# Kernel optimization log

Measured on AMD Instinct MI355X. Metric: run time of the kernel, lower is better.

The kernel has to match this reference:

```python
import jax, jax.numpy as jnp
import numpy as np

B = 64                      # batch_size: number of candidate elements
N_PER = 100_000             # observations per candidate
DATA = B * N_PER            # data_size
EPS = 1e-6
INV_ROOT_2PI = 1.0 / np.sqrt(2.0 * np.pi)

def _deg2dist(deg):
    # chord distance on unit sphere subtended by angle deg
    return 2.0 * np.sin(np.radians(deg) / 2.0)

THRESH_DEG = 1.0
THRESH_S2_MIN = np.float32(_deg2dist(10.0 / 3600.0) ** 2)
THRESH_S2_MAX = np.float32(_deg2dist(THRESH_DEG) ** 2)
LOG_THRESH_S2_RANGE = np.float32(np.log(THRESH_S2_MAX / THRESH_S2_MIN))


def setup_inputs() -> dict:
    key = jax.random.key(0)
    k1, k2, k3, k4, k5 = jax.random.split(key, 5)
    u_obs = jax.random.normal(k1, (DATA, 3), dtype=jnp.float32)
    u_obs = u_obs / jnp.linalg.norm(u_obs, axis=-1, keepdims=True)   # unit directions
    # predicted directions = observed + small perturbation so some obs fall inside threshold
    u_pred = u_obs + 0.01 * jax.random.normal(k2, (DATA, 3), dtype=jnp.float32)
    u_pred = u_pred / jnp.linalg.norm(u_pred, axis=-1, keepdims=True)
    mag_obs = 18.0 + jax.random.normal(k3, (DATA,), dtype=jnp.float32)
    R_elt = 0.001 + 0.004 * jax.random.uniform(k4, (B,), dtype=jnp.float32)  # resolution param
    thresh_s2_ = jax.random.uniform(k5, (B,), dtype=jnp.float32)             # trainable, in [0,1]
    seg_ids = jnp.repeat(jnp.arange(B, dtype=jnp.int32), N_PER)              # ragged row_lengths -> segment ids
    return {"u_pred": u_pred, "R_elt": R_elt, "u_obs": u_obs,
            "mag_obs": mag_obs, "thresh_s2_": thresh_s2_, "seg_ids": seg_ids}


def reference(u_pred, R_elt, u_obs, mag_obs, thresh_s2_, seg_ids):
    # threshold transform (get_thresh_s2)
    thresh_s2_elt = THRESH_S2_MIN * jnp.exp(thresh_s2_ * LOG_THRESH_S2_RANGE)    # [B]
    thresh_all = thresh_s2_elt[seg_ids]                                          # [DATA]

    # calc_dist: squared chord distance + threshold mask
    du = u_pred - u_obs
    s2 = jnp.sum(du * du, axis=-1)                                               # [DATA]
    is_close = s2 < thresh_all                                                   # bool [DATA]
    mask = is_close.astype(s2.dtype)
    v = s2 / thresh_all                                                          # in [0,1] on close obs

    # cond_pdf_dist: exponential-family pdf conditional on a hit (q_miss = 1)
    lam_elt = 0.5 * thresh_s2_elt / (R_elt * R_elt)                              # [B]
    lam = lam_elt[seg_ids]                                                       # [DATA]
    log_q_hit = -lam * v + jnp.log(lam) - jnp.log1p(-jnp.exp(-lam))              # log(e^{-lam v} lam / (1 - e^{-lam}))

    # mag_standardize: per-candidate mean/std over close observations -> z-score
    n_close = jax.ops.segment_sum(mask, seg_ids, num_segments=B, indices_are_sorted=True)
    n_safe = jnp.maximum(n_close, 1.0)
    sum_m = jax.ops.segment_sum(mask * mag_obs, seg_ids, num_segments=B, indices_are_sorted=True)
    sum_m2 = jax.ops.segment_sum(mask * mag_obs * mag_obs, seg_ids, num_segments=B, indices_are_sorted=True)
    mu = sum_m / n_safe                                                          # [B]
    var = jnp.maximum(sum_m2 / n_safe - mu * mu, EPS)
    sigma_hat = jnp.sqrt(var)                                                    # [B]

    z = (mag_obs - mu[seg_ids]) / sigma_hat[seg_ids]                             # [DATA]
    log_p_mag = jnp.log(INV_ROOT_2PI / sigma_hat[seg_ids]) - 0.5 * z * z

    # per-candidate score: segment-sum of log conditional densities on close obs
    score = jax.ops.segment_sum(mask * (log_q_hit + log_p_mag), seg_ids,
                                num_segments=B, indices_are_sorted=True)         # [B]
    return score
```

## Files before the change

kernel.cpp:

```cpp
#include <hip/hip_runtime.h>
#include <math.h>


#define BLOCK 128
#define WAVES (BLOCK / 64)
#define SEG_BLOCKS 16
#define WAVES_PER_SEG (SEG_BLOCKS * WAVES)
#define OBS_PER_ITER 256
#define BUF_FLOATS 1792
#define WAVE_LDS (2 * BUF_FLOATS)

typedef const __attribute__((address_space(1))) unsigned int g_u32;
typedef __attribute__((address_space(3))) unsigned int l_u32;

__device__ __forceinline__ void ld_lds16(const float* g, float* l) {
    __builtin_amdgcn_global_load_lds((g_u32*)g, (l_u32*)l, 16, 0, 0);
}

__global__ __launch_bounds__(BLOCK, 2) void ts_main_kernel(
    const float* __restrict__ u_pred,
    const float* __restrict__ u_obs,
    const float* __restrict__ mag,
    const float* __restrict__ thresh_raw,
    float* __restrict__ acc,
    int n_per, float ts_min, float log_range)
{
    __shared__ float lds[WAVES * WAVE_LDS];

    const int seg  = blockIdx.x / SEG_BLOCKS;
    const int cid  = blockIdx.x % SEG_BLOCKS;
    const int widx = threadIdx.x >> 6;
    const int lane = threadIdx.x & 63;
    const int wv   = cid * WAVES + widx;

    float* wlds = &lds[widx * WAVE_LDS];

    const long long segO = (long long)seg * n_per;
    const float* predBase = u_pred + segO * 3;
    const float* obsBase  = u_obs  + segO * 3;
    const float* magBase  = mag + segO;

    const int  niter  = (n_per + OBS_PER_ITER - 1) / OBS_PER_ITER;
    const long long dirMax = (long long)n_per * 3 - 4;
    const long long magMax = (long long)n_per - 4;

    const float thresh = ts_min * expf(thresh_raw[seg] * log_range);

    auto stage = [&](int buf, int it) {
        float* b = wlds + buf * BUF_FLOATS;
        const long long fbase = (long long)it * 768;
        #pragma unroll
        for (int c = 0; c < 3; ++c) {
            long long fo = fbase + c * 256 + lane * 4;
            if (fo > dirMax) fo = dirMax;
            ld_lds16(predBase + fo, b + c * 256);
        }
        #pragma unroll
        for (int c = 0; c < 3; ++c) {
            long long fo = fbase + c * 256 + lane * 4;
            if (fo > dirMax) fo = dirMax;
            ld_lds16(obsBase + fo, b + 768 + c * 256);
        }
        long long mo = (long long)it * 256 + lane * 4;
        if (mo > magMax) mo = magMax;
        ld_lds16(magBase + mo, b + 1536);
    };

    float cnt = 0.f, sm = 0.f, sm2 = 0.f, ss2 = 0.f;

    int it = wv;
    if (it < niter) stage(0, it);

    int t = 0;
    for (; it < niter; it += WAVES_PER_SEG, ++t) {
        const int nxt = it + WAVES_PER_SEG;
        const int cur = t & 1;
        if (nxt < niter) {
            stage(cur ^ 1, nxt);
            asm volatile("s_waitcnt vmcnt(7)" ::: "memory");
        } else {
            asm volatile("s_waitcnt vmcnt(0)" ::: "memory");
        }

        const float* b = wlds + cur * BUF_FLOATS;
        const float4 p0 = *reinterpret_cast<const float4*>(b + 12 * lane);
        const float4 p1 = *reinterpret_cast<const float4*>(b + 12 * lane + 4);
        const float4 p2 = *reinterpret_cast<const float4*>(b + 12 * lane + 8);
        const float4 o0 = *reinterpret_cast<const float4*>(b + 768 + 12 * lane);
        const float4 o1 = *reinterpret_cast<const float4*>(b + 768 + 12 * lane + 4);
        const float4 o2 = *reinterpret_cast<const float4*>(b + 768 + 12 * lane + 8);
        const float4 mg = *reinterpret_cast<const float4*>(b + 1536 + 4 * lane);

        const bool valid = (it * OBS_PER_ITER + lane * 4) < n_per;

        float s2[4];
        {
            float dx, dy, dz;
            dx = p0.x-o0.x; dy = p0.y-o0.y; dz = p0.z-o0.z; s2[0] = dx*dx+dy*dy+dz*dz;
            dx = p0.w-o0.w; dy = p1.x-o1.x; dz = p1.y-o1.y; s2[1] = dx*dx+dy*dy+dz*dz;
            dx = p1.z-o1.z; dy = p1.w-o1.w; dz = p2.x-o2.x; s2[2] = dx*dx+dy*dy+dz*dz;
            dx = p2.y-o2.y; dy = p2.z-o2.z; dz = p2.w-o2.w; s2[3] = dx*dx+dy*dy+dz*dz;
        }
        const float m[4] = {mg.x, mg.y, mg.z, mg.w};
        #pragma unroll
        for (int i = 0; i < 4; ++i) {
            const bool cl = valid && (s2[i] < thresh);
            if (cl) { cnt += 1.f; sm += m[i]; sm2 += m[i]*m[i]; ss2 += s2[i]; }
        }
    }

    for (int off = 32; off > 0; off >>= 1) {
        cnt += __shfl_down(cnt, off);
        sm  += __shfl_down(sm,  off);
        sm2 += __shfl_down(sm2, off);
        ss2 += __shfl_down(ss2, off);
    }
    if (lane == 0 && cnt != 0.f) {
        atomicAdd(&acc[seg * 4 + 0], cnt);
        atomicAdd(&acc[seg * 4 + 1], sm);
        atomicAdd(&acc[seg * 4 + 2], sm2);
        atomicAdd(&acc[seg * 4 + 3], ss2);
    }
}

__global__ void ts_final_kernel(
    const float* __restrict__ acc,
    const float* __restrict__ R_elt,
    const float* __restrict__ thresh_raw,
    float* __restrict__ out,
    int Bn, float ts_min, float log_range)
{
    const int b = blockIdx.x * blockDim.x + threadIdx.x;
    if (b >= Bn) return;

    const float n   = acc[b * 4 + 0];
    const float sm  = acc[b * 4 + 1];
    const float sm2 = acc[b * 4 + 2];
    const float ss2 = acc[b * 4 + 3];

    float score = 0.f;
    if (n > 0.f) {
        const float thresh = ts_min * expf(thresh_raw[b] * log_range);
        const float R   = R_elt[b];
        const float lam = 0.5f * thresh / (R * R);
        const float C   = logf(lam) - logf(-expm1f(-lam));

        const float ssd     = sm2 - sm * (sm / n);
        const float var_raw = ssd / n;
        const float var     = fmaxf(var_raw, 1e-6f);
        const float sigma   = sqrtf(var);
        const float log_inv_root_2pi = -0.9189385332046727f;

        score = -lam * (ss2 / thresh)
              + n * C
              + n * (log_inv_root_2pi - logf(sigma))
              - 0.5f * (ssd / var);
    }
    out[b] = score;
}

extern "C" void kernel_launch(void* const* d_in, const int* in_sizes, int n_in,
                              void* d_out, int out_size, void* d_ws, size_t ws_size,
                              hipStream_t stream) {
    const float* u_pred     = (const float*)d_in[0];
    const float* R_elt      = (const float*)d_in[1];
    const float* u_obs      = (const float*)d_in[2];
    const float* mag_obs    = (const float*)d_in[3];
    const float* thresh_raw = (const float*)d_in[4];

    const int B     = in_sizes[1];
    const int DATA  = in_sizes[3];
    const int n_per = DATA / B;

    float* acc = (float*)d_ws;
    float* out = (float*)d_out;

    const double rad_min = M_PI / 180.0 * (10.0 / 3600.0);
    const double rad_max = M_PI / 180.0 * 1.0;
    const float ts_min = (float)((2.0 * sin(rad_min / 2.0)) * (2.0 * sin(rad_min / 2.0)));
    const float ts_max = (float)((2.0 * sin(rad_max / 2.0)) * (2.0 * sin(rad_max / 2.0)));
    const float log_range = logf(ts_max / ts_min);

    hipMemsetAsync(acc, 0, (size_t)B * 4 * sizeof(float), stream);

    ts_main_kernel<<<B * SEG_BLOCKS, BLOCK, 0, stream>>>(
        u_pred, u_obs, mag_obs, thresh_raw, acc, n_per, ts_min, log_range);

    ts_final_kernel<<<1, 64, 0, stream>>>(
        acc, R_elt, thresh_raw, out, B, ts_min, log_range);
}
```

Baseline: 43.53 us.

## Use single-wave blocks with triple-buffered LDS prefetch pipeline

Blocks shrink from two waves to one, and each segment now gets 28 blocks instead of 16. The per-wave LDS staging moves from double to triple buffering, so two iterations of global-to-LDS loads are in flight before each compute step. The aim is to hide more HBM latency and raise the number of waves streaming memory on this bandwidth-bound reduction. In exchange it adds more atomics per segment and more LDS per wave, which may limit occupancy. It also assumes wv < niter, since the first stage is issued unconditionally.

```diff
diff --git a/kernel.cpp b/kernel.cpp
--- a/kernel.cpp
+++ b/kernel.cpp
@@ -2,13 +2,12 @@
 #include <math.h>
 
 
-#define BLOCK 128
-#define WAVES (BLOCK / 64)
-#define SEG_BLOCKS 16
-#define WAVES_PER_SEG (SEG_BLOCKS * WAVES)
+#define BLOCK 64
+#define SEG_BLOCKS 28
+#define WPSEG SEG_BLOCKS
 #define OBS_PER_ITER 256
 #define BUF_FLOATS 1792
-#define WAVE_LDS (2 * BUF_FLOATS)
+#define DEPTH 3
 
 typedef const __attribute__((address_space(1))) unsigned int g_u32;
 typedef __attribute__((address_space(3))) unsigned int l_u32;
@@ -25,29 +24,25 @@
     float* __restrict__ acc,
     int n_per, float ts_min, float log_range)
 {
-    __shared__ float lds[WAVES * WAVE_LDS];
+    __shared__ float lds[DEPTH * BUF_FLOATS];
 
     const int seg  = blockIdx.x / SEG_BLOCKS;
-    const int cid  = blockIdx.x % SEG_BLOCKS;
-    const int widx = threadIdx.x >> 6;
+    const int wv   = blockIdx.x % SEG_BLOCKS;
     const int lane = threadIdx.x & 63;
-    const int wv   = cid * WAVES + widx;
-
-    float* wlds = &lds[widx * WAVE_LDS];
 
     const long long segO = (long long)seg * n_per;
     const float* predBase = u_pred + segO * 3;
     const float* obsBase  = u_obs  + segO * 3;
     const float* magBase  = mag + segO;
 
-    const int  niter  = (n_per + OBS_PER_ITER - 1) / OBS_PER_ITER;
+    const int niter = (n_per + OBS_PER_ITER - 1) / OBS_PER_ITER;
     const long long dirMax = (long long)n_per * 3 - 4;
     const long long magMax = (long long)n_per - 4;
 
     const float thresh = ts_min * expf(thresh_raw[seg] * log_range);
 
     auto stage = [&](int buf, int it) {
-        float* b = wlds + buf * BUF_FLOATS;
+        float* b = &lds[buf * BUF_FLOATS];
         const long long fbase = (long long)it * 768;
         #pragma unroll
         for (int c = 0; c < 3; ++c) {
@@ -68,44 +63,51 @@
 
     float cnt = 0.f, sm = 0.f, sm2 = 0.f, ss2 = 0.f;
 
-    int it = wv;
-    if (it < niter) stage(0, it);
+    {
+        const int it0 = wv;
+        stage(0, it0);
+        if (it0 + WPSEG < niter) stage(1, it0 + WPSEG);
 
-    int t = 0;
-    for (; it < niter; it += WAVES_PER_SEG, ++t) {
-        const int nxt = it + WAVES_PER_SEG;
-        const int cur = t & 1;
-        if (nxt < niter) {
-            stage(cur ^ 1, nxt);
-            asm volatile("s_waitcnt vmcnt(7)" ::: "memory");
-        } else {
-            asm volatile("s_waitcnt vmcnt(0)" ::: "memory");
-        }
+        int buf = 0;
+        int it  = it0;
+        for (; it < niter; it += WPSEG) {
+            const int it2 = it + 2 * WPSEG;
+            if (it2 < niter) {
+                stage((buf + 2) % DEPTH, it2);
+                asm volatile("s_waitcnt vmcnt(14)" ::: "memory");
+            } else if (it + WPSEG < niter) {
+                asm volatile("s_waitcnt vmcnt(7)" ::: "memory");
+            } else {
+                asm volatile("s_waitcnt vmcnt(0)" ::: "memory");
+            }
 
-        const float* b = wlds + cur * BUF_FLOATS;
-        const float4 p0 = *reinterpret_cast<const float4*>(b + 12 * lane);
-        const float4 p1 = *reinterpret_cast<const float4*>(b + 12 * lane + 4);
-        const float4 p2 = *reinterpret_cast<const float4*>(b + 12 * lane + 8);
-        const float4 o0 = *reinterpret_cast<const float4*>(b + 768 + 12 * lane);
-        const float4 o1 = *reinterpret_cast<const float4*>(b + 768 + 12 * lane + 4);
-        const float4 o2 = *reinterpret_cast<const float4*>(b + 768 + 12 * lane + 8);
-        const float4 mg = *reinterpret_cast<const float4*>(b + 1536 + 4 * lane);
+            const float* b = &lds[buf * BUF_FLOATS];
+            const float4 p0 = *reinterpret_cast<const float4*>(b + 12 * lane);
+            const float4 p1 = *reinterpret_cast<const float4*>(b + 12 * lane + 4);
+            const float4 p2 = *reinterpret_cast<const float4*>(b + 12 * lane + 8);
+            const float4 o0 = *reinterpret_cast<const float4*>(b + 768 + 12 * lane);
+            const float4 o1 = *reinterpret_cast<const float4*>(b + 768 + 12 * lane + 4);
+            const float4 o2 = *reinterpret_cast<const float4*>(b + 768 + 12 * lane + 8);
+            const float4 mg = *reinterpret_cast<const float4*>(b + 1536 + 4 * lane);
 
-        const bool valid = (it * OBS_PER_ITER + lane * 4) < n_per;
+            const bool valid = (it * OBS_PER_ITER + lane * 4) < n_per;
 
-        float s2[4];
-        {
-            float dx, dy, dz;
-            dx = p0.x-o0.x; dy = p0.y-o0.y; dz = p0.z-o0.z; s2[0] = dx*dx+dy*dy+dz*dz;
-            dx = p0.w-o0.w; dy = p1.x-o1.x; dz = p1.y-o1.y; s2[1] = dx*dx+dy*dy+dz*dz;
-            dx = p1.z-o1.z; dy = p1.w-o1.w; dz = p2.x-o2.x; s2[2] = dx*dx+dy*dy+dz*dz;
-            dx = p2.y-o2.y; dy = p2.z-o2.z; dz = p2.w-o2.w; s2[3] = dx*dx+dy*dy+dz*dz;
-        }
-        const float m[4] = {mg.x, mg.y, mg.z, mg.w};
-        #pragma unroll
-        for (int i = 0; i < 4; ++i) {
-            const bool cl = valid && (s2[i] < thresh);
-            if (cl) { cnt += 1.f; sm += m[i]; sm2 += m[i]*m[i]; ss2 += s2[i]; }
+            float s2[4];
+            {
+                float dx, dy, dz;
+                dx = p0.x-o0.x; dy = p0.y-o0.y; dz = p0.z-o0.z; s2[0] = dx*dx+dy*dy+dz*dz;
+                dx = p0.w-o0.w; dy = p1.x-o1.x; dz = p1.y-o1.y; s2[1] = dx*dx+dy*dy+dz*dz;
+                dx = p1.z-o1.z; dy = p1.w-o1.w; dz = p2.x-o2.x; s2[2] = dx*dx+dy*dy+dz*dz;
+                dx = p2.y-o2.y; dy = p2.z-o2.z; dz = p2.w-o2.w; s2[3] = dx*dx+dy*dy+dz*dz;
+            }
+            const float m[4] = {mg.x, mg.y, mg.z, mg.w};
+            #pragma unroll
+            for (int i = 0; i < 4; ++i) {
+                const bool cl = valid && (s2[i] < thresh);
+                if (cl) { cnt += 1.f; sm += m[i]; sm2 += m[i]*m[i]; ss2 += s2[i]; }
+            }
+
+            buf = (buf + 1) % DEPTH;
         }
     }
 
```

After: 43.80 us. Within noise of the previous version (+0.6%).
